# Performance work log

Hardware: AMD Instinct MI355X
Metric: run time of the kernel (lower is better)

## Reference

```python
import jax, jax.numpy as jnp
import numpy as np

# Mamba2 hyperparameters (from init_kwargs + mamba_ssm defaults)
D_MODEL = 1024
D_STATE = 64
D_CONV = 4
EXPAND = 2
HEADDIM = 64                      # mamba_ssm default
D_INNER = EXPAND * D_MODEL        # 2048
NHEADS = D_INNER // HEADDIM       # 32
NGROUPS = 1
CONV_DIM = D_INNER + 2 * NGROUPS * D_STATE      # 2176
D_IN_PROJ = 2 * D_INNER + 2 * NGROUPS * D_STATE + NHEADS  # 4256
BATCH, SEQLEN = 4, 2048


def setup_inputs() -> dict:
    key = jax.random.key(0)
    ks = jax.random.split(key, 8)
    x = jax.random.normal(ks[0], (BATCH, SEQLEN, D_MODEL), dtype=jnp.float32)
    W_in = jax.random.normal(ks[1], (D_MODEL, D_IN_PROJ), dtype=jnp.float32) * 0.02
    conv_w = jax.random.normal(ks[2], (CONV_DIM, D_CONV), dtype=jnp.float32) * 0.2
    conv_b = jnp.zeros((CONV_DIM,), dtype=jnp.float32)
    # dt_bias = inverse-softplus of dt ~ U(1e-3, 0.1), as in mamba_ssm init
    dt = jnp.exp(jax.random.uniform(ks[3], (NHEADS,)) * (np.log(0.1) - np.log(1e-3)) + np.log(1e-3))
    dt_bias = dt + jnp.log(-jnp.expm1(-dt))
    A_log = jnp.log(jax.random.uniform(ks[4], (NHEADS,), minval=1.0, maxval=16.0))
    D = jnp.ones((NHEADS,), dtype=jnp.float32)
    norm_w = jnp.ones((D_INNER,), dtype=jnp.float32)
    W_out = jax.random.normal(ks[5], (D_INNER, D_MODEL), dtype=jnp.float32) * 0.02
    return {"x": x, "W_in": W_in, "conv_w": conv_w, "conv_b": conv_b,
            "dt_bias": dt_bias, "A_log": A_log, "D": D, "norm_w": norm_w, "W_out": W_out}


def _mamba2_forward(x, W_in, conv_w, conv_b, dt_bias, A_log, D, norm_w, W_out):
    Bsz, L, _ = x.shape
    zxbcdt = x @ W_in                                   # [B, L, D_IN_PROJ]
    z = zxbcdt[..., :D_INNER]                           # gate
    xBC = zxbcdt[..., D_INNER:D_INNER + CONV_DIM]
    dt = zxbcdt[..., D_INNER + CONV_DIM:]               # [B, L, H]
    dt = jax.nn.softplus(dt + dt_bias)

    # causal depthwise conv1d over time, kernel width D_CONV
    xp = jnp.pad(xBC, ((0, 0), (D_CONV - 1, 0), (0, 0)))
    xc = sum(xp[:, k:k + L, :] * conv_w[:, k] for k in range(D_CONV))
    xBC = jax.nn.silu(xc + conv_b)

    xh = xBC[..., :D_INNER].reshape(Bsz, L, NHEADS, HEADDIM)   # [B,L,H,P]
    Bm = xBC[..., D_INNER:D_INNER + D_STATE]                   # [B,L,N] (ngroups=1)
    Cm = xBC[..., D_INNER + D_STATE:]                          # [B,L,N]
    A = -jnp.exp(A_log)                                        # [H]

    # selective SSM scan: h_t = h_{t-1}*exp(dt_t*A) + dt_t * x_t (outer) B_t ; y_t = C_t . h_t
    def step(h, inp):
        dt_t, x_t, B_t, C_t = inp                 # [B,H],[B,H,P],[B,N],[B,N]
        dA = jnp.exp(dt_t * A)                    # [B,H]
        h = h * dA[..., None, None] + (dt_t[..., None] * x_t)[..., None] * B_t[:, None, None, :]
        y_t = jnp.einsum('bhpn,bn->bhp', h, C_t)
        return h, y_t

    h0 = jnp.zeros((Bsz, NHEADS, HEADDIM, D_STATE), dtype=x.dtype)
    inputs = (jnp.moveaxis(dt, 1, 0), jnp.moveaxis(xh, 1, 0),
              jnp.moveaxis(Bm, 1, 0), jnp.moveaxis(Cm, 1, 0))
    _, ys = jax.lax.scan(step, h0, inputs)                     # [L,B,H,P]
    y = jnp.moveaxis(ys, 0, 1) + xh * D[None, None, :, None]   # skip term D*x
    y = y.reshape(Bsz, L, D_INNER)

    # gated RMSNorm: norm(y * silu(z)) * weight
    y = y * jax.nn.silu(z)
    y = y * jax.lax.rsqrt(jnp.mean(y * y, axis=-1, keepdims=True) + 1e-5) * norm_w
    return y @ W_out


def reference(x, W_in, conv_w, conv_b, dt_bias, A_log, D, norm_w, W_out):
    return _mamba2_forward(x, W_in, conv_w, conv_b, dt_bias, A_log, D, norm_w, W_out)
```

## Files before the change

kernel.cpp:

```cpp
#include <hip/hip_runtime.h>
#include <hip/hip_bf16.h>

#define B_SZ   4
#define SEQ    2048
#define DM     1024
#define DIN    2048
#define DST    64
#define NH     32
#define HD     64
#define CONVD  2176
#define DPROJ  4256
#define NPAD1  4352
#define MROWS  (B_SZ*SEQ)
#define QC     64
#define NC     (SEQ/QC)


typedef __attribute__((ext_vector_type(8))) __bf16 bf16x8;
typedef __attribute__((ext_vector_type(4))) __bf16 bf16x4;
typedef __attribute__((ext_vector_type(4))) float  floatx4;

__device__ __forceinline__ int swz(int row, int col) {
    return row * 64 + ((((col >> 3) ^ (row & 7)) << 3) | (col & 7));
}
__device__ __forceinline__ float bfbits2f(unsigned short u) {
    return __uint_as_float(((unsigned int)u) << 16);
}
__device__ __forceinline__ unsigned short f2bfbits(float f) {
    union { __bf16 h; unsigned short u; } cv; cv.h = (__bf16)f; return cv.u;
}

__global__ __launch_bounds__(256) void dtw_prep_kernel(const float* __restrict__ W_in,
                                                       float* __restrict__ dtWc) {
    int idx = blockIdx.x * 256 + threadIdx.x;
    int k = idx >> 5, h = idx & 31;
    dtWc[idx] = W_in[(size_t)k * DPROJ + 2 * DIN + 2 * DST + h];
}

__global__ __launch_bounds__(256) void cvt_dt_kernel(const float* __restrict__ x,
                                                     const float* __restrict__ dtWc,
                                                     __bf16* __restrict__ xbf,
                                                     float* __restrict__ dtraw) {
    __shared__ float xs[16][132];
    __shared__ float dtw[128 * 32];
    const int tid = threadIdx.x;
    const int r0 = blockIdx.x * 16;
    const int lm = tid & 15, pos = tid >> 4;
    const int rr = tid >> 4, h2 = (tid & 15) * 2;
    __bf16* slab = xbf + (size_t)blockIdx.x * (16 * DM);

    float a0 = 0.f, a1 = 0.f;
    for (int kc = 0; kc < 8; kc++) {
        #pragma unroll
        for (int i = 0; i < 2; i++) {
            int idx = tid + 256 * i;
            int row = idx >> 5, c4 = idx & 31;
            float4 v = ((const float4*)(x + (size_t)(r0 + row) * DM + kc * 128))[c4];
            xs[row][c4 * 4 + 0] = v.x; xs[row][c4 * 4 + 1] = v.y;
            xs[row][c4 * 4 + 2] = v.z; xs[row][c4 * 4 + 3] = v.w;
        }
        #pragma unroll
        for (int i = 0; i < 16; i++)
            dtw[tid + 256 * i] = dtWc[kc * 4096 + tid + 256 * i];
        __syncthreads();
        {
            bf16x8 o;
            #pragma unroll
            for (int e = 0; e < 8; e++) o[e] = (__bf16)xs[lm][pos * 8 + e];
            int kb = kc * 4 + (pos >> 2), q = pos & 3;
            *(bf16x8*)(slab + (size_t)(kb * 64 + q * 16 + lm) * 8) = o;
        }
        for (int j = 0; j < 128; j++) {
            float xv = xs[rr][j];
            a0 = fmaf(xv, dtw[j * 32 + h2], a0);
            a1 = fmaf(xv, dtw[j * 32 + h2 + 1], a1);
        }
        __syncthreads();
    }
    dtraw[(size_t)(r0 + rr) * NH + h2]     = a0;
    dtraw[(size_t)(r0 + rr) * NH + h2 + 1] = a1;
}

__global__ __launch_bounds__(256) void transpose_tiled_kernel(const float* __restrict__ src,
                                                              __bf16* __restrict__ dst,
                                                              int Ksrc, int Csrc) {
    __shared__ float tile[32][129];
    const int tid = threadIdx.x;
    const int mb = blockIdx.x, kb = blockIdx.y;
    const int K32 = Ksrc >> 5;
    #pragma unroll
    for (int i = 0; i < 4; i++) {
        int idx = tid + 256 * i;
        int kl = idx >> 5, c4 = idx & 31;
        int n = mb * 128 + c4 * 4;
        float4 v = make_float4(0.f, 0.f, 0.f, 0.f);
        if (n < Csrc) v = *(const float4*)(src + (size_t)(kb * 32 + kl) * Csrc + n);
        tile[kl][c4 * 4 + 0] = v.x; tile[kl][c4 * 4 + 1] = v.y;
        tile[kl][c4 * 4 + 2] = v.z; tile[kl][c4 * 4 + 3] = v.w;
    }
    __syncthreads();
    #pragma unroll
    for (int i = 0; i < 2; i++) {
        int c = tid + 256 * i;
        int sub = c >> 6, ln = c & 63, q = ln >> 4, lmn = ln & 15;
        bf16x8 o;
        #pragma unroll
        for (int e = 0; e < 8; e++) o[e] = (__bf16)tile[q * 8 + e][sub * 16 + lmn];
        *(bf16x8*)(dst + ((((size_t)(mb * 8 + sub)) * K32 + kb) << 9) + (ln << 3)) = o;
    }
}

template<int STORE_BF16>
__global__ __launch_bounds__(256) void gemm_tt_kernel(const __bf16* __restrict__ A,
                                                      const __bf16* __restrict__ Bt,
                                                      float* __restrict__ Cf,
                                                      __bf16* __restrict__ Cb,
                                                      int N, int K) {
    __shared__ __align__(16) __bf16 As[4096];
    __shared__ __align__(16) __bf16 Bs[4096];
    const int tid = threadIdx.x;
    const int wave = tid >> 6, lane = tid & 63;
    const int lm = lane & 15, lq = lane >> 4;
    const int mb = blockIdx.x, nb = blockIdx.y;
    const int K32 = K >> 5;

    floatx4 acc[4][4] = {};

    for (int kb = 0; kb < K32; kb++) {
        #pragma unroll
        for (int r = 0; r < 2; r++) {
            int c = tid + (r << 8);
            int sub = c >> 6, ln = c & 63;
            __builtin_amdgcn_global_load_lds(
                reinterpret_cast<const unsigned int*>(
                    A + ((((size_t)(mb * 8 + sub)) * K32 + kb) << 9) + (ln << 3)),
                reinterpret_cast<unsigned int*>(As + (size_t)c * 8), 16, 0, 0);
            __builtin_amdgcn_global_load_lds(
                reinterpret_cast<const unsigned int*>(
                    Bt + ((((size_t)(nb * 8 + sub)) * K32 + kb) << 9) + (ln << 3)),
                reinterpret_cast<unsigned int*>(Bs + (size_t)c * 8), 16, 0, 0);
        }
        __syncthreads();
        bf16x8 af[4], bfr[4];
        #pragma unroll
        for (int i = 0; i < 4; i++)
            af[i] = *(const bf16x8*)(As + ((((wave & 1) << 2) + i) << 9) + (lane << 3));
        #pragma unroll
        for (int i = 0; i < 4; i++)
            bfr[i] = *(const bf16x8*)(Bs + ((((wave >> 1) << 2) + i) << 9) + (lane << 3));
        #pragma unroll
        for (int mi = 0; mi < 4; mi++)
            #pragma unroll
            for (int ni = 0; ni < 4; ni++)
                acc[mi][ni] = __builtin_amdgcn_mfma_f32_16x16x32_bf16(af[mi], bfr[ni], acc[mi][ni], 0, 0, 0);
        __syncthreads();
    }

    const int wm = (wave & 1) << 6, wn = (wave >> 1) << 6;
    #pragma unroll
    for (int mi = 0; mi < 4; mi++) {
        #pragma unroll
        for (int r = 0; r < 4; r++) {
            int row = mb * 128 + wm + mi * 16 + lq * 4 + r;
            #pragma unroll
            for (int ni = 0; ni < 4; ni++) {
                int col = nb * 128 + wn + ni * 16 + lm;
                if (col < N) {
                    if (STORE_BF16) Cb[(size_t)row * N + col] = (__bf16)acc[mi][ni][r];
                    else            Cf[(size_t)row * N + col] = acc[mi][ni][r];
                }
            }
        }
    }
}

__global__ __launch_bounds__(256) void conv_silu_kernel(const __bf16* __restrict__ zx,
                                                        const float* __restrict__ cw,
                                                        const float* __restrict__ cb,
                                                        __bf16* __restrict__ out) {
    const int tid = threadIdx.x;
    const int tc = tid & 15, tt = tid >> 4;
    const int c0 = (blockIdx.x * 16 + tc) * 8;
    const int tg = blockIdx.y * 16 + tt;
    const int b = tg >> 8, t0 = (tg & 255) << 3;

    float xb[11][8];
    #pragma unroll
    for (int i = 0; i < 11; i++) {
        int t = t0 + i - 3;
        if (t >= 0) {
            bf16x8 v = *(const bf16x8*)(zx + ((size_t)(b * SEQ + t)) * DPROJ + DIN + c0);
            #pragma unroll
            for (int j = 0; j < 8; j++) xb[i][j] = (float)v[j];
        } else {
            #pragma unroll
            for (int j = 0; j < 8; j++) xb[i][j] = 0.f;
        }
    }
    float w0[8], w1[8], w2[8], w3[8], bias[8];
    #pragma unroll
    for (int j = 0; j < 8; j++) {
        float4 w = *(const float4*)(cw + (size_t)(c0 + j) * 4);
        w0[j] = w.x; w1[j] = w.y; w2[j] = w.z; w3[j] = w.w;
        bias[j] = cb[c0 + j];
    }
    #pragma unroll
    for (int s = 0; s < 8; s++) {
        bf16x8 o;
        #pragma unroll
        for (int j = 0; j < 8; j++) {
            float v = bias[j] + w0[j] * xb[s][j] + w1[j] * xb[s + 1][j]
                              + w2[j] * xb[s + 2][j] + w3[j] * xb[s + 3][j];
            o[j] = (__bf16)(v / (1.f + __expf(-v)));
        }
        *(bf16x8*)(out + ((size_t)(b * SEQ + t0 + s)) * CONVD + c0) = o;
    }
}

__global__ __launch_bounds__(256) void dt_prep_kernel(const float* __restrict__ dtraw,
                                                      const float* __restrict__ dt_bias,
                                                      const float* __restrict__ A_log,
                                                      float* __restrict__ dtv,
                                                      float* __restrict__ cum) {
    int blk = blockIdx.x;
    int b = blk >> 5, h = blk & 31;
    int wave = threadIdx.x >> 6, lane = threadIdx.x & 63;
    float Ah = -__expf(A_log[h]);
    float dtb = dt_bias[h];
    for (int c = wave; c < NC; c += 4) {
        int t = c * QC + lane;
        float u = dtraw[((size_t)b * SEQ + t) * NH + h] + dtb;
        float d = fmaxf(u, 0.f) + log1pf(__expf(-fabsf(u)));
        float s = d * Ah;
        #pragma unroll
        for (int o = 1; o < 64; o <<= 1) {
            float v = __shfl_up(s, o);
            if (lane >= o) s += v;
        }
        size_t idx = (size_t)blk * SEQ + t;
        dtv[idx] = d;
        cum[idx] = s;
    }
}

__global__ __launch_bounds__(256) void chunk_state_kernel(const __bf16* __restrict__ xc,
                                                          const float* __restrict__ dtv,
                                                          const float* __restrict__ cum,
                                                          __bf16* __restrict__ Sbuf) {
    const int blk = blockIdx.x;
    const int hq = blk & 7;
    const int bc = blk >> 3;
    const int c = bc & (NC - 1), b = bc >> 5;
    const int tid = threadIdx.x;
    const int wave = tid >> 6, lane = tid & 63;
    const int lm = lane & 15, q = lane >> 4;
    const int h = hq * 4 + wave;

    __shared__ __align__(16) __bf16 sBt[4096];
    __shared__ __align__(16) __bf16 sXw[4][4096];

    const size_t rowbase = (size_t)b * SEQ + (size_t)c * QC;
    {
        int k = tid & 31, n0 = (tid >> 5) * 8;
        unsigned short u0[8], u1[8];
        *(uint4*)u0 = *(const uint4*)(xc + (rowbase + 2 * k) * CONVD + DIN + n0);
        *(uint4*)u1 = *(const uint4*)(xc + (rowbase + 2 * k + 1) * CONVD + DIN + n0);
        #pragma unroll
        for (int i = 0; i < 8; i++) {
            unsigned int v = (unsigned int)u0[i] | ((unsigned int)u1[i] << 16);
            ((unsigned int*)sBt)[swz(n0 + i, 2 * k) >> 1] = v;
        }
    }
    const float* cump = cum + (size_t)(b * NH + h) * SEQ + (size_t)c * QC;
    const float* dtp  = dtv + (size_t)(b * NH + h) * SEQ + (size_t)c * QC;
    {
        int k = lane & 31, ph = (lane >> 5) * 32;
        float clast = cump[63];
        float w0 = dtp[2 * k]     * __expf(clast - cump[2 * k]);
        float w1 = dtp[2 * k + 1] * __expf(clast - cump[2 * k + 1]);
        unsigned short u0[32], u1[32];
        const __bf16* r0 = xc + (rowbase + 2 * k) * CONVD + h * 64 + ph;
        const __bf16* r1 = xc + (rowbase + 2 * k + 1) * CONVD + h * 64 + ph;
        #pragma unroll
        for (int i = 0; i < 4; i++) {
            ((uint4*)u0)[i] = ((const uint4*)r0)[i];
            ((uint4*)u1)[i] = ((const uint4*)r1)[i];
        }
        unsigned int* dstw = (unsigned int*)sXw[wave];
        #pragma unroll
        for (int i = 0; i < 32; i++) {
            unsigned int lo = f2bfbits(bfbits2f(u0[i]) * w0);
            unsigned int hi = f2bfbits(bfbits2f(u1[i]) * w1);
            dstw[swz(ph + i, 2 * k) >> 1] = lo | (hi << 16);
        }
    }
    __syncthreads();

    floatx4 acc[4][4] = {};
    #pragma unroll
    for (int kb = 0; kb < 2; kb++) {
        bf16x8 aX[4], bB[4];
        #pragma unroll
        for (int pi = 0; pi < 4; pi++)
            aX[pi] = *(const bf16x8*)(&sXw[wave][swz(pi * 16 + lm, kb * 32 + q * 8)]);
        #pragma unroll
        for (int ni = 0; ni < 4; ni++)
            bB[ni] = *(const bf16x8*)(&sBt[swz(ni * 16 + lm, kb * 32 + q * 8)]);
        #pragma unroll
        for (int pi = 0; pi < 4; pi++)
            #pragma unroll
            for (int ni = 0; ni < 4; ni++)
                acc[pi][ni] = __builtin_amdgcn_mfma_f32_16x16x32_bf16(aX[pi], bB[ni], acc[pi][ni], 0, 0, 0);
    }
    __bf16* Sp = Sbuf + ((size_t)(b * NC + c) * NH + h) * (HD * DST);
    #pragma unroll
    for (int pi = 0; pi < 4; pi++)
        #pragma unroll
        for (int r = 0; r < 4; r++) {
            int p = pi * 16 + q * 4 + r;
            #pragma unroll
            for (int ni = 0; ni < 4; ni++)
                Sp[p * 64 + ni * 16 + lm] = (__bf16)acc[pi][ni][r];
        }
}

__global__ __launch_bounds__(256) void state_scan_kernel(__bf16* __restrict__ Sbuf,
                                                         const float* __restrict__ cum) {
    int blk = blockIdx.x;
    int b = blk >> 5, h = blk & 31;
    int off = threadIdx.x * 16;
    float run[16];
    #pragma unroll
    for (int n = 0; n < 16; n++) run[n] = 0.f;
    for (int c = 0; c < NC; c++) {
        __bf16* Sp = Sbuf + ((size_t)(b * NC + c) * NH + h) * (HD * DST) + off;
        float tmp[16];
        #pragma unroll
        for (int n = 0; n < 16; n++) tmp[n] = (float)Sp[n];
        #pragma unroll
        for (int n = 0; n < 16; n++) Sp[n] = (__bf16)run[n];
        float P = __expf(cum[(size_t)blk * SEQ + c * QC + QC - 1]);
        #pragma unroll
        for (int n = 0; n < 16; n++) run[n] = fmaf(run[n], P, tmp[n]);
    }
}

__global__ __launch_bounds__(128) void chunk_out_kernel(const __bf16* __restrict__ xc,
                                                        const float* __restrict__ dtv,
                                                        const float* __restrict__ cum,
                                                        const __bf16* __restrict__ Sbuf,
                                                        const float* __restrict__ Dv,
                                                        __bf16* __restrict__ y) {
    const int blk = blockIdx.x;
    const int hp = blk & 15;
    const int bc = blk >> 4;
    const int c = bc & (NC - 1), b = bc >> 5;
    const int tid = threadIdx.x;
    const int wave = tid >> 6, lane = tid & 63;
    const int lm = lane & 15, q = lane >> 4;
    const int h = hp * 2 + wave;

    __shared__ __align__(16) __bf16 smem[16384];
    __bf16* sB  = smem;
    __bf16* sC  = smem + 4096;
    __bf16* sXt = smem + 8192 + (wave << 12);
    __bf16* sP  = smem + (wave << 12);

    const size_t rowbase = (size_t)b * SEQ + (size_t)c * QC;
    {
        int r = tid >> 1, c0 = (tid & 1) * 32;
        const __bf16* gB = xc + (rowbase + r) * CONVD + DIN + c0;
        const __bf16* gC = xc + (rowbase + r) * CONVD + DIN + DST + c0;
        #pragma unroll
        for (int i = 0; i < 4; i++) {
            *(uint4*)(&sB[swz(r, c0 + i * 8)]) = *(const uint4*)(gB + i * 8);
            *(uint4*)(&sC[swz(r, c0 + i * 8)]) = *(const uint4*)(gC + i * 8);
        }
    }
    {
        int k = lane & 31, ph = (lane >> 5) * 32;
        unsigned short u0[32], u1[32];
        const __bf16* r0 = xc + (rowbase + 2 * k) * CONVD + h * 64 + ph;
        const __bf16* r1 = xc + (rowbase + 2 * k + 1) * CONVD + h * 64 + ph;
        #pragma unroll
        for (int i = 0; i < 4; i++) {
            ((uint4*)u0)[i] = ((const uint4*)r0)[i];
            ((uint4*)u1)[i] = ((const uint4*)r1)[i];
        }
        unsigned int* dstw = (unsigned int*)sXt;
        #pragma unroll
        for (int i = 0; i < 32; i++)
            dstw[swz(ph + i, 2 * k) >> 1] = (unsigned int)u0[i] | ((unsigned int)u1[i] << 16);
    }
    __syncthreads();

    const float* cump = cum + (size_t)(b * NH + h) * SEQ + (size_t)c * QC;
    const float* dtp  = dtv + (size_t)(b * NH + h) * SEQ + (size_t)c * QC;
    float cumv = cump[lane], dtvv = dtp[lane];
    float ct[4][4];
    #pragma unroll
    for (int ti = 0; ti < 4; ti++)
        #pragma unroll
        for (int r = 0; r < 4; r++)
            ct[ti][r] = __shfl(cumv, ti * 16 + q * 4 + r);
    float cums_l[4], dtv_l[4];
    #pragma unroll
    for (int si = 0; si < 4; si++) {
        cums_l[si] = __shfl(cumv, si * 16 + lm);
        dtv_l[si]  = __shfl(dtvv, si * 16 + lm);
    }

    bf16x8 afC[4][2];
    #pragma unroll
    for (int ti = 0; ti < 4; ti++)
        #pragma unroll
        for (int kb = 0; kb < 2; kb++)
            afC[ti][kb] = *(const bf16x8*)(&sC[swz(ti * 16 + lm, kb * 32 + q * 8)]);

    floatx4 accG[4][4] = {};
    #pragma unroll
    for (int kb = 0; kb < 2; kb++) {
        bf16x8 bfB[4];
        #pragma unroll
        for (int si = 0; si < 4; si++)
            bfB[si] = *(const bf16x8*)(&sB[swz(si * 16 + lm, kb * 32 + q * 8)]);
        #pragma unroll
        for (int ti = 0; ti < 4; ti++)
            #pragma unroll
            for (int si = 0; si < 4; si++)
                if (si <= ti)
                    accG[ti][si] = __builtin_amdgcn_mfma_f32_16x16x32_bf16(afC[ti][kb], bfB[si], accG[ti][si], 0, 0, 0);
    }
    __syncthreads();

    float Dh = Dv[h];
    #pragma unroll
    for (int ti = 0; ti < 4; ti++)
        #pragma unroll
        for (int si = 0; si < 4; si++) {
            if (si > ti) continue;
            #pragma unroll
            for (int r = 0; r < 4; r++) {
                int t = ti * 16 + q * 4 + r;
                float arg = fminf(ct[ti][r] - cums_l[si], 0.f);
                float val = dtv_l[si] * __expf(arg) * accG[ti][si][r];
                if (ti == si) {
                    if (lm > q * 4 + r) val = 0.f;
                    else if (lm == q * 4 + r) val += Dh;
                }
                sP[swz(t, si * 16 + lm)] = (__bf16)val;
            }
        }
    #pragma unroll
    for (int r = 0; r < 4; r++) {
        sP[swz(q * 4 + r, 16 + lm)] = (__bf16)0.f;
        sP[swz(32 + q * 4 + r, 48 + lm)] = (__bf16)0.f;
    }
    __syncthreads();

    floatx4 accY[4][4] = {};
    const __bf16* Sp = Sbuf + ((size_t)(b * NC + c) * NH + h) * (HD * DST);
    #pragma unroll
    for (int kb = 0; kb < 2; kb++) {
        bf16x8 bS[4];
        #pragma unroll
        for (int pi = 0; pi < 4; pi++)
            bS[pi] = *(const bf16x8*)(Sp + (pi * 16 + lm) * 64 + kb * 32 + q * 8);
        #pragma unroll
        for (int ti = 0; ti < 4; ti++)
            #pragma unroll
            for (int pi = 0; pi < 4; pi++)
                accY[ti][pi] = __builtin_amdgcn_mfma_f32_16x16x32_bf16(afC[ti][kb], bS[pi], accY[ti][pi], 0, 0, 0);
    }
    #pragma unroll
    for (int ti = 0; ti < 4; ti++)
        #pragma unroll
        for (int r = 0; r < 4; r++) {
            float e = __expf(ct[ti][r]);
            #pragma unroll
            for (int pi = 0; pi < 4; pi++)
                accY[ti][pi][r] *= e;
        }

    #pragma unroll
    for (int kb = 0; kb < 2; kb++) {
        bf16x8 bX[4];
        #pragma unroll
        for (int pi = 0; pi < 4; pi++)
            bX[pi] = *(const bf16x8*)(&sXt[swz(pi * 16 + lm, kb * 32 + q * 8)]);
        #pragma unroll
        for (int ti = 0; ti < 4; ti++) {
            if (ti < 2 * kb) continue;
            bf16x8 aP = *(const bf16x8*)(&sP[swz(ti * 16 + lm, kb * 32 + q * 8)]);
            #pragma unroll
            for (int pi = 0; pi < 4; pi++)
                accY[ti][pi] = __builtin_amdgcn_mfma_f32_16x16x32_bf16(aP, bX[pi], accY[ti][pi], 0, 0, 0);
        }
    }

    const int R4v = (int)(rowbase >> 4);
    #pragma unroll
    for (int ti = 0; ti < 4; ti++) {
        __bf16* slab = y + (size_t)(R4v + ti) * 32768;
        #pragma unroll
        for (int pi = 0; pi < 4; pi++) {
            int kbC = h * 2 + (pi >> 1);
            int qC  = ((pi & 1) << 1) + (lm >> 3);
            int colpart = kbC * 512 + qC * 128 + (lm & 7);
            #pragma unroll
            for (int r = 0; r < 4; r++)
                slab[colpart + (q * 4 + r) * 8] = (__bf16)accY[ti][pi][r];
        }
    }
}

__global__ __launch_bounds__(256) void gate_norm_kernel(__bf16* __restrict__ y,
                                                        const __bf16* __restrict__ zx,
                                                        const float* __restrict__ nw) {
    const int tid = threadIdx.x;
    const int lm = tid & 15;
    __bf16* yfb = y + (size_t)blockIdx.x * 32768;
    const size_t zrow = ((size_t)blockIdx.x * 16 + lm) * DPROJ;

    float ss = 0.f;
    #pragma unroll
    for (int i = 0; i < 16; i++) {
        int g = tid + 256 * i;
        int pos = g >> 4;
        bf16x8 yv = *(const bf16x8*)(yfb + (size_t)g * 8);
        bf16x8 zv = *(const bf16x8*)(zx + zrow + pos * 8);
        #pragma unroll
        for (int j = 0; j < 8; j++) {
            float z = (float)zv[j];
            float val = (float)yv[j] * (z / (1.f + __expf(-z)));
            ss += val * val;
        }
    }
    __shared__ float red[16][16];
    __shared__ float sscale[16];
    red[lm][tid >> 4] = ss;
    __syncthreads();
    if (tid < 16) {
        float tot = 0.f;
        #pragma unroll
        for (int j = 0; j < 16; j++) tot += red[tid][j];
        sscale[tid] = rsqrtf(tot * (1.f / (float)DIN) + 1e-5f);
    }
    __syncthreads();
    float sc = sscale[lm];
    #pragma unroll
    for (int i = 0; i < 16; i++) {
        int g = tid + 256 * i;
        int pos = g >> 4;
        bf16x8 yv = *(const bf16x8*)(yfb + (size_t)g * 8);
        bf16x8 zv = *(const bf16x8*)(zx + zrow + pos * 8);
        float4 n0 = *(const float4*)(nw + pos * 8);
        float4 n1 = *(const float4*)(nw + pos * 8 + 4);
        float nwv[8] = {n0.x, n0.y, n0.z, n0.w, n1.x, n1.y, n1.z, n1.w};
        bf16x8 o;
        #pragma unroll
        for (int j = 0; j < 8; j++) {
            float z = (float)zv[j];
            float val = (float)yv[j] * (z / (1.f + __expf(-z)));
            o[j] = (__bf16)(val * sc * nwv[j]);
        }
        *(bf16x8*)(yfb + (size_t)g * 8) = o;
    }
}

extern "C" void kernel_launch(void* const* d_in, const int* in_sizes, int n_in,
                              void* d_out, int out_size, void* d_ws, size_t ws_size,
                              hipStream_t stream) {
    const float* x       = (const float*)d_in[0];
    const float* W_in    = (const float*)d_in[1];
    const float* conv_w  = (const float*)d_in[2];
    const float* conv_b  = (const float*)d_in[3];
    const float* dt_bias = (const float*)d_in[4];
    const float* A_log   = (const float*)d_in[5];
    const float* Dv      = (const float*)d_in[6];
    const float* norm_w  = (const float*)d_in[7];
    const float* W_out   = (const float*)d_in[8];
    float* out = (float*)d_out;

    char* ws = (char*)d_ws;
    size_t off = 0;
    auto take = [&](size_t bytes) { void* p = ws + off; off = (off + bytes + 255) & ~(size_t)255; return p; };
    __bf16* xbf    = (__bf16*)take((size_t)MROWS * DM * 2);
    __bf16* WinT   = (__bf16*)take((size_t)NPAD1 * DM * 2);
    __bf16* WoutT  = (__bf16*)take((size_t)DM * DIN * 2);
    __bf16* zx     = (__bf16*)take((size_t)MROWS * DPROJ * 2);
    __bf16* xc     = (__bf16*)take((size_t)MROWS * CONVD * 2);
    __bf16* yf     = (__bf16*)take((size_t)MROWS * DIN * 2);
    float*  dtraw  = (float*) take((size_t)MROWS * NH * 4);
    float*  dtv    = (float*) take((size_t)B_SZ * NH * SEQ * 4);
    float*  cum    = (float*) take((size_t)B_SZ * NH * SEQ * 4);
    __bf16* Sbuf   = (__bf16*)take((size_t)B_SZ * NC * NH * HD * DST * 2);
    float*  dtWc   = (float*) take((size_t)DM * NH * 4);
    (void)ws_size;

    dtw_prep_kernel<<<dim3(DM * NH / 256), 256, 0, stream>>>(W_in, dtWc);
    cvt_dt_kernel<<<dim3(MROWS / 16), 256, 0, stream>>>(x, dtWc, xbf, dtraw);
    transpose_tiled_kernel<<<dim3(NPAD1 / 128, DM / 32), 256, 0, stream>>>(W_in, WinT, DM, DPROJ);
    transpose_tiled_kernel<<<dim3(DM / 128, DIN / 32), 256, 0, stream>>>(W_out, WoutT, DIN, DM);
    gemm_tt_kernel<1><<<dim3(MROWS / 128, NPAD1 / 128), 256, 0, stream>>>(
        xbf, WinT, nullptr, zx, DPROJ, DM);
    conv_silu_kernel<<<dim3(17, 64), 256, 0, stream>>>(zx, conv_w, conv_b, xc);
    dt_prep_kernel<<<dim3(B_SZ * NH), 256, 0, stream>>>(dtraw, dt_bias, A_log, dtv, cum);
    chunk_state_kernel<<<dim3(B_SZ * NC * (NH / 4)), 256, 0, stream>>>(xc, dtv, cum, Sbuf);
    state_scan_kernel<<<dim3(B_SZ * NH), 256, 0, stream>>>(Sbuf, cum);
    chunk_out_kernel<<<dim3(B_SZ * NC * (NH / 2)), 128, 0, stream>>>(xc, dtv, cum, Sbuf, Dv, yf);
    gate_norm_kernel<<<dim3(MROWS / 16), 256, 0, stream>>>(yf, zx, norm_w);
    gemm_tt_kernel<0><<<dim3(MROWS / 128, DM / 128), 256, 0, stream>>>(
        yf, WoutT, out, nullptr, DM, DIN);
}
```

Before: 402.9 us.

## Fuse gated RMSNorm into chunk output and GEMM epilogue, merge prep kernels

Removes the separate gate_norm pass. chunk_out now applies silu(z) gating, writes the gated y, and atomically accumulates per-row sums of squares. The output GEMM epilogue applies the rsqrt row scale, and norm_w is folded into the transposed W_out during weight prep. The two weight transposes and the dt-weight extraction become one kernel, conv and dt_prep merge into one launch that also zeroes rowsum, and the in_proj GEMM drops the dt columns (N 4352→4224), since dt is already computed separately. state_scan splits each head across 4 blocks with vectorized bf16x4 access. The cost is atomics and uncoalesced z reads in chunk_out.

Result: faster. 379.6 us (-5.8%).

```diff
diff --git a/kernel.cpp b/kernel.cpp
--- a/kernel.cpp
+++ b/kernel.cpp
@@ -10,7 +10,7 @@
 #define HD     64
 #define CONVD  2176
 #define DPROJ  4256
-#define NPAD1  4352
+#define NPROJ  4224
 #define MROWS  (B_SZ*SEQ)
 #define QC     64
 #define NC     (SEQ/QC)
@@ -30,11 +30,50 @@
     union { __bf16 h; unsigned short u; } cv; cv.h = (__bf16)f; return cv.u;
 }
 
-__global__ __launch_bounds__(256) void dtw_prep_kernel(const float* __restrict__ W_in,
-                                                       float* __restrict__ dtWc) {
-    int idx = blockIdx.x * 256 + threadIdx.x;
-    int k = idx >> 5, h = idx & 31;
-    dtWc[idx] = W_in[(size_t)k * DPROJ + 2 * DIN + 2 * DST + h];
+__global__ __launch_bounds__(256) void prep_weights_kernel(const float* __restrict__ W_in,
+                                                           const float* __restrict__ W_out,
+                                                           const float* __restrict__ norm_w,
+                                                           float* __restrict__ dtWc,
+                                                           __bf16* __restrict__ WinT,
+                                                           __bf16* __restrict__ WoutT) {
+    __shared__ float tile[32][129];
+    const int bid = blockIdx.x, tid = threadIdx.x;
+    if (bid < 128) {
+        int idx = bid * 256 + tid;
+        int k = idx >> 5, h = idx & 31;
+        dtWc[idx] = W_in[(size_t)k * DPROJ + 2 * DIN + 2 * DST + h];
+        return;
+    }
+    const float* src; __bf16* dst; const float* scal; int Ksrc, Csrc, mb, kb;
+    if (bid < 128 + 1056) {
+        int t = bid - 128; mb = t >> 5; kb = t & 31;
+        src = W_in; dst = WinT; scal = nullptr; Ksrc = DM; Csrc = DPROJ;
+    } else {
+        int t = bid - 1184; mb = t >> 6; kb = t & 63;
+        src = W_out; dst = WoutT; scal = norm_w; Ksrc = DIN; Csrc = DM;
+    }
+    const int K32 = Ksrc >> 5;
+    #pragma unroll
+    for (int i = 0; i < 4; i++) {
+        int idx = tid + 256 * i;
+        int kl = idx >> 5, c4 = idx & 31;
+        int n = mb * 128 + c4 * 4;
+        float4 v = make_float4(0.f, 0.f, 0.f, 0.f);
+        if (n < Csrc) v = *(const float4*)(src + (size_t)(kb * 32 + kl) * Csrc + n);
+        if (scal) { float s = scal[kb * 32 + kl]; v.x *= s; v.y *= s; v.z *= s; v.w *= s; }
+        tile[kl][c4 * 4 + 0] = v.x; tile[kl][c4 * 4 + 1] = v.y;
+        tile[kl][c4 * 4 + 2] = v.z; tile[kl][c4 * 4 + 3] = v.w;
+    }
+    __syncthreads();
+    #pragma unroll
+    for (int i = 0; i < 2; i++) {
+        int c = tid + 256 * i;
+        int sub = c >> 6, ln = c & 63, q = ln >> 4, lmn = ln & 15;
+        bf16x8 o;
+        #pragma unroll
+        for (int e = 0; e < 8; e++) o[e] = (__bf16)tile[q * 8 + e][sub * 16 + lmn];
+        *(bf16x8*)(dst + ((((size_t)(mb * 8 + sub)) * K32 + kb) << 9) + (ln << 3)) = o;
+    }
 }
 
 __global__ __launch_bounds__(256) void cvt_dt_kernel(const float* __restrict__ x,
@@ -81,40 +120,12 @@
     dtraw[(size_t)(r0 + rr) * NH + h2 + 1] = a1;
 }
 
-__global__ __launch_bounds__(256) void transpose_tiled_kernel(const float* __restrict__ src,
-                                                              __bf16* __restrict__ dst,
-                                                              int Ksrc, int Csrc) {
-    __shared__ float tile[32][129];
-    const int tid = threadIdx.x;
-    const int mb = blockIdx.x, kb = blockIdx.y;
-    const int K32 = Ksrc >> 5;
-    #pragma unroll
-    for (int i = 0; i < 4; i++) {
-        int idx = tid + 256 * i;
-        int kl = idx >> 5, c4 = idx & 31;
-        int n = mb * 128 + c4 * 4;
-        float4 v = make_float4(0.f, 0.f, 0.f, 0.f);
-        if (n < Csrc) v = *(const float4*)(src + (size_t)(kb * 32 + kl) * Csrc + n);
-        tile[kl][c4 * 4 + 0] = v.x; tile[kl][c4 * 4 + 1] = v.y;
-        tile[kl][c4 * 4 + 2] = v.z; tile[kl][c4 * 4 + 3] = v.w;
-    }
-    __syncthreads();
-    #pragma unroll
-    for (int i = 0; i < 2; i++) {
-        int c = tid + 256 * i;
-        int sub = c >> 6, ln = c & 63, q = ln >> 4, lmn = ln & 15;
-        bf16x8 o;
-        #pragma unroll
-        for (int e = 0; e < 8; e++) o[e] = (__bf16)tile[q * 8 + e][sub * 16 + lmn];
-        *(bf16x8*)(dst + ((((size_t)(mb * 8 + sub)) * K32 + kb) << 9) + (ln << 3)) = o;
-    }
-}
-
 template<int STORE_BF16>
 __global__ __launch_bounds__(256) void gemm_tt_kernel(const __bf16* __restrict__ A,
                                                       const __bf16* __restrict__ Bt,
                                                       float* __restrict__ Cf,
                                                       __bf16* __restrict__ Cb,
+                                                      const float* __restrict__ rowscale,
                                                       int N, int K) {
     __shared__ __align__(16) __bf16 As[4096];
     __shared__ __align__(16) __bf16 Bs[4096];
@@ -162,84 +173,92 @@
         #pragma unroll
         for (int r = 0; r < 4; r++) {
             int row = mb * 128 + wm + mi * 16 + lq * 4 + r;
+            float s = 1.f;
+            if (rowscale) s = rsqrtf(rowscale[row] * (1.f / (float)DIN) + 1e-5f);
             #pragma unroll
             for (int ni = 0; ni < 4; ni++) {
                 int col = nb * 128 + wn + ni * 16 + lm;
                 if (col < N) {
                     if (STORE_BF16) Cb[(size_t)row * N + col] = (__bf16)acc[mi][ni][r];
-                    else            Cf[(size_t)row * N + col] = acc[mi][ni][r];
+                    else            Cf[(size_t)row * N + col] = acc[mi][ni][r] * s;
                 }
             }
         }
     }
 }
 
-__global__ __launch_bounds__(256) void conv_silu_kernel(const __bf16* __restrict__ zx,
-                                                        const float* __restrict__ cw,
-                                                        const float* __restrict__ cb,
-                                                        __bf16* __restrict__ out) {
-    const int tid = threadIdx.x;
-    const int tc = tid & 15, tt = tid >> 4;
-    const int c0 = (blockIdx.x * 16 + tc) * 8;
-    const int tg = blockIdx.y * 16 + tt;
-    const int b = tg >> 8, t0 = (tg & 255) << 3;
-
-    float xb[11][8];
-    #pragma unroll
-    for (int i = 0; i < 11; i++) {
-        int t = t0 + i - 3;
-        if (t >= 0) {
-            bf16x8 v = *(const bf16x8*)(zx + ((size_t)(b * SEQ + t)) * DPROJ + DIN + c0);
-            #pragma unroll
-            for (int j = 0; j < 8; j++) xb[i][j] = (float)v[j];
-        } else {
-            #pragma unroll
-            for (int j = 0; j < 8; j++) xb[i][j] = 0.f;
-        }
-    }
-    float w0[8], w1[8], w2[8], w3[8], bias[8];
-    #pragma unroll
-    for (int j = 0; j < 8; j++) {
-        float4 w = *(const float4*)(cw + (size_t)(c0 + j) * 4);
-        w0[j] = w.x; w1[j] = w.y; w2[j] = w.z; w3[j] = w.w;
-        bias[j] = cb[c0 + j];
-    }
-    #pragma unroll
-    for (int s = 0; s < 8; s++) {
-        bf16x8 o;
-        #pragma unroll
-        for (int j = 0; j < 8; j++) {
-            float v = bias[j] + w0[j] * xb[s][j] + w1[j] * xb[s + 1][j]
-                              + w2[j] * xb[s + 2][j] + w3[j] * xb[s + 3][j];
-            o[j] = (__bf16)(v / (1.f + __expf(-v)));
-        }
-        *(bf16x8*)(out + ((size_t)(b * SEQ + t0 + s)) * CONVD + c0) = o;
-    }
-}
-
-__global__ __launch_bounds__(256) void dt_prep_kernel(const float* __restrict__ dtraw,
+__global__ __launch_bounds__(256) void conv_dt_kernel(const __bf16* __restrict__ zx,
+                                                      const float* __restrict__ cw,
+                                                      const float* __restrict__ cb,
+                                                      __bf16* __restrict__ out,
+                                                      const float* __restrict__ dtraw,
                                                       const float* __restrict__ dt_bias,
                                                       const float* __restrict__ A_log,
                                                       float* __restrict__ dtv,
-                                                      float* __restrict__ cum) {
-    int blk = blockIdx.x;
-    int b = blk >> 5, h = blk & 31;
-    int wave = threadIdx.x >> 6, lane = threadIdx.x & 63;
-    float Ah = -__expf(A_log[h]);
-    float dtb = dt_bias[h];
-    for (int c = wave; c < NC; c += 4) {
-        int t = c * QC + lane;
-        float u = dtraw[((size_t)b * SEQ + t) * NH + h] + dtb;
-        float d = fmaxf(u, 0.f) + log1pf(__expf(-fabsf(u)));
-        float s = d * Ah;
-        #pragma unroll
-        for (int o = 1; o < 64; o <<= 1) {
-            float v = __shfl_up(s, o);
-            if (lane >= o) s += v;
-        }
-        size_t idx = (size_t)blk * SEQ + t;
-        dtv[idx] = d;
-        cum[idx] = s;
+                                                      float* __restrict__ cum,
+                                                      float* __restrict__ rowsum) {
+    const int bid = blockIdx.x, tid = threadIdx.x;
+    if (bid < 1088) {
+        const int by = bid / 17, bx = bid - by * 17;
+        const int tc = tid & 15, tt = tid >> 4;
+        const int c0 = (bx * 16 + tc) * 8;
+        const int tg = by * 16 + tt;
+        const int b = tg >> 8, t0 = (tg & 255) << 3;
+
+        float xb[11][8];
+        #pragma unroll
+        for (int i = 0; i < 11; i++) {
+            int t = t0 + i - 3;
+            if (t >= 0) {
+                bf16x8 v = *(const bf16x8*)(zx + ((size_t)(b * SEQ + t)) * NPROJ + DIN + c0);
+                #pragma unroll
+                for (int j = 0; j < 8; j++) xb[i][j] = (float)v[j];
+            } else {
+                #pragma unroll
+                for (int j = 0; j < 8; j++) xb[i][j] = 0.f;
+            }
+        }
+        float w0[8], w1[8], w2[8], w3[8], bias[8];
+        #pragma unroll
+        for (int j = 0; j < 8; j++) {
+            float4 w = *(const float4*)(cw + (size_t)(c0 + j) * 4);
+            w0[j] = w.x; w1[j] = w.y; w2[j] = w.z; w3[j] = w.w;
+            bias[j] = cb[c0 + j];
+        }
+        #pragma unroll
+        for (int s = 0; s < 8; s++) {
+            bf16x8 o;
+            #pragma unroll
+            for (int j = 0; j < 8; j++) {
+                float v = bias[j] + w0[j] * xb[s][j] + w1[j] * xb[s + 1][j]
+                                  + w2[j] * xb[s + 2][j] + w3[j] * xb[s + 3][j];
+                o[j] = (__bf16)(v / (1.f + __expf(-v)));
+            }
+            *(bf16x8*)(out + ((size_t)(b * SEQ + t0 + s)) * CONVD + c0) = o;
+        }
+    } else if (bid < 1216) {
+        const int blk = bid - 1088;
+        const int b = blk >> 5, h = blk & 31;
+        const int wave = tid >> 6, lane = tid & 63;
+        float Ah = -__expf(A_log[h]);
+        float dtb = dt_bias[h];
+        for (int c = wave; c < NC; c += 4) {
+            int t = c * QC + lane;
+            float u = dtraw[((size_t)b * SEQ + t) * NH + h] + dtb;
+            float d = fmaxf(u, 0.f) + log1pf(__expf(-fabsf(u)));
+            float s = d * Ah;
+            #pragma unroll
+            for (int o = 1; o < 64; o <<= 1) {
+                float v = __shfl_up(s, o);
+                if (lane >= o) s += v;
+            }
+            size_t idx = (size_t)blk * SEQ + t;
+            dtv[idx] = d;
+            cum[idx] = s;
+        }
+    } else {
+        float4 z = make_float4(0.f, 0.f, 0.f, 0.f);
+        *(float4*)(rowsum + (size_t)(bid - 1216) * 1024 + tid * 4) = z;
     }
 }
 
@@ -326,22 +345,26 @@
 
 __global__ __launch_bounds__(256) void state_scan_kernel(__bf16* __restrict__ Sbuf,
                                                          const float* __restrict__ cum) {
-    int blk = blockIdx.x;
+    int blk = blockIdx.x >> 2;
+    int part = blockIdx.x & 3;
     int b = blk >> 5, h = blk & 31;
-    int off = threadIdx.x * 16;
-    float run[16];
-    #pragma unroll
-    for (int n = 0; n < 16; n++) run[n] = 0.f;
+    int off = part * 1024 + threadIdx.x * 4;
+    float run[4];
+    #pragma unroll
+    for (int n = 0; n < 4; n++) run[n] = 0.f;
     for (int c = 0; c < NC; c++) {
         __bf16* Sp = Sbuf + ((size_t)(b * NC + c) * NH + h) * (HD * DST) + off;
-        float tmp[16];
-        #pragma unroll
-        for (int n = 0; n < 16; n++) tmp[n] = (float)Sp[n];
-        #pragma unroll
-        for (int n = 0; n < 16; n++) Sp[n] = (__bf16)run[n];
+        bf16x4 sv = *(const bf16x4*)Sp;
+        float tmp[4];
+        #pragma unroll
+        for (int n = 0; n < 4; n++) tmp[n] = (float)sv[n];
+        bf16x4 ov;
+        #pragma unroll
+        for (int n = 0; n < 4; n++) ov[n] = (__bf16)run[n];
+        *(bf16x4*)Sp = ov;
         float P = __expf(cum[(size_t)blk * SEQ + c * QC + QC - 1]);
         #pragma unroll
-        for (int n = 0; n < 16; n++) run[n] = fmaf(run[n], P, tmp[n]);
+        for (int n = 0; n < 4; n++) run[n] = fmaf(run[n], P, tmp[n]);
     }
 }
 
@@ -350,6 +373,8 @@
                                                         const float* __restrict__ cum,
                                                         const __bf16* __restrict__ Sbuf,
                                                         const float* __restrict__ Dv,
+                                                        const __bf16* __restrict__ zx,
+                                                        float* __restrict__ rowsum,
                                                         __bf16* __restrict__ y) {
     const int blk = blockIdx.x;
     const int hp = blk & 15;
@@ -503,68 +528,25 @@
     for (int ti = 0; ti < 4; ti++) {
         __bf16* slab = y + (size_t)(R4v + ti) * 32768;
         #pragma unroll
-        for (int pi = 0; pi < 4; pi++) {
-            int kbC = h * 2 + (pi >> 1);
-            int qC  = ((pi & 1) << 1) + (lm >> 3);
-            int colpart = kbC * 512 + qC * 128 + (lm & 7);
-            #pragma unroll
-            for (int r = 0; r < 4; r++)
-                slab[colpart + (q * 4 + r) * 8] = (__bf16)accY[ti][pi][r];
-        }
-    }
-}
-
-__global__ __launch_bounds__(256) void gate_norm_kernel(__bf16* __restrict__ y,
-                                                        const __bf16* __restrict__ zx,
-                                                        const float* __restrict__ nw) {
-    const int tid = threadIdx.x;
-    const int lm = tid & 15;
-    __bf16* yfb = y + (size_t)blockIdx.x * 32768;
-    const size_t zrow = ((size_t)blockIdx.x * 16 + lm) * DPROJ;
-
-    float ss = 0.f;
-    #pragma unroll
-    for (int i = 0; i < 16; i++) {
-        int g = tid + 256 * i;
-        int pos = g >> 4;
-        bf16x8 yv = *(const bf16x8*)(yfb + (size_t)g * 8);
-        bf16x8 zv = *(const bf16x8*)(zx + zrow + pos * 8);
-        #pragma unroll
-        for (int j = 0; j < 8; j++) {
-            float z = (float)zv[j];
-            float val = (float)yv[j] * (z / (1.f + __expf(-z)));
-            ss += val * val;
-        }
-    }
-    __shared__ float red[16][16];
-    __shared__ float sscale[16];
-    red[lm][tid >> 4] = ss;
-    __syncthreads();
-    if (tid < 16) {
-        float tot = 0.f;
-        #pragma unroll
-        for (int j = 0; j < 16; j++) tot += red[tid][j];
-        sscale[tid] = rsqrtf(tot * (1.f / (float)DIN) + 1e-5f);
-    }
-    __syncthreads();
-    float sc = sscale[lm];
-    #pragma unroll
-    for (int i = 0; i < 16; i++) {
-        int g = tid + 256 * i;
-        int pos = g >> 4;
-        bf16x8 yv = *(const bf16x8*)(yfb + (size_t)g * 8);
-        bf16x8 zv = *(const bf16x8*)(zx + zrow + pos * 8);
-        float4 n0 = *(const float4*)(nw + pos * 8);
-        float4 n1 = *(const float4*)(nw + pos * 8 + 4);
-        float nwv[8] = {n0.x, n0.y, n0.z, n0.w, n1.x, n1.y, n1.z, n1.w};
-        bf16x8 o;
-        #pragma unroll
-        for (int j = 0; j < 8; j++) {
-            float z = (float)zv[j];
-            float val = (float)yv[j] * (z / (1.f + __expf(-z)));
-            o[j] = (__bf16)(val * sc * nwv[j]);
-        }
-        *(bf16x8*)(yfb + (size_t)g * 8) = o;
+        for (int r = 0; r < 4; r++) {
+            int t = ti * 16 + q * 4 + r;
+            const __bf16* zrow = zx + (rowbase + t) * NPROJ + h * 64;
+            float rs = 0.f;
+            #pragma unroll
+            for (int pi = 0; pi < 4; pi++) {
+                float zv = (float)zrow[pi * 16 + lm];
+                float g = accY[ti][pi][r] * (zv / (1.f + __expf(-zv)));
+                rs += g * g;
+                int kbC = h * 2 + (pi >> 1);
+                int qC  = ((pi & 1) << 1) + (lm >> 3);
+                slab[kbC * 512 + qC * 128 + (lm & 7) + (q * 4 + r) * 8] = (__bf16)g;
+            }
+            rs += __shfl_xor(rs, 1);
+            rs += __shfl_xor(rs, 2);
+            rs += __shfl_xor(rs, 4);
+            rs += __shfl_xor(rs, 8);
+            if (lm == 0) atomicAdd(&rowsum[rowbase + t], rs);
+        }
     }
 }
 
@@ -586,9 +568,9 @@
     size_t off = 0;
     auto take = [&](size_t bytes) { void* p = ws + off; off = (off + bytes + 255) & ~(size_t)255; return p; };
     __bf16* xbf    = (__bf16*)take((size_t)MROWS * DM * 2);
-    __bf16* WinT   = (__bf16*)take((size_t)NPAD1 * DM * 2);
+    __bf16* WinT   = (__bf16*)take((size_t)NPROJ * DM * 2);
     __bf16* WoutT  = (__bf16*)take((size_t)DM * DIN * 2);
-    __bf16* zx     = (__bf16*)take((size_t)MROWS * DPROJ * 2);
+    __bf16* zx     = (__bf16*)take((size_t)MROWS * NPROJ * 2);
     __bf16* xc     = (__bf16*)take((size_t)MROWS * CONVD * 2);
     __bf16* yf     = (__bf16*)take((size_t)MROWS * DIN * 2);
     float*  dtraw  = (float*) take((size_t)MROWS * NH * 4);
@@ -596,20 +578,19 @@
     float*  cum    = (float*) take((size_t)B_SZ * NH * SEQ * 4);
     __bf16* Sbuf   = (__bf16*)take((size_t)B_SZ * NC * NH * HD * DST * 2);
     float*  dtWc   = (float*) take((size_t)DM * NH * 4);
+    float*  rowsum = (float*) take((size_t)MROWS * 4);
     (void)ws_size;
 
-    dtw_prep_kernel<<<dim3(DM * NH / 256), 256, 0, stream>>>(W_in, dtWc);
+    prep_weights_kernel<<<dim3(1696), 256, 0, stream>>>(W_in, W_out, norm_w, dtWc, WinT, WoutT);
     cvt_dt_kernel<<<dim3(MROWS / 16), 256, 0, stream>>>(x, dtWc, xbf, dtraw);
-    transpose_tiled_kernel<<<dim3(NPAD1 / 128, DM / 32), 256, 0, stream>>>(W_in, WinT, DM, DPROJ);
-    transpose_tiled_kernel<<<dim3(DM / 128, DIN / 32), 256, 0, stream>>>(W_out, WoutT, DIN, DM);
-    gemm_tt_kernel<1><<<dim3(MROWS / 128, NPAD1 / 128), 256, 0, stream>>>(
-        xbf, WinT, nullptr, zx, DPROJ, DM);
-    conv_silu_kernel<<<dim3(17, 64), 256, 0, stream>>>(zx, conv_w, conv_b, xc);
-    dt_prep_kernel<<<dim3(B_SZ * NH), 256, 0, stream>>>(dtraw, dt_bias, A_log, dtv, cum);
+    gemm_tt_kernel<1><<<dim3(MROWS / 128, NPROJ / 128), 256, 0, stream>>>(
+        xbf, WinT, nullptr, zx, nullptr, NPROJ, DM);
+    conv_dt_kernel<<<dim3(1224), 256, 0, stream>>>(zx, conv_w, conv_b, xc,
+                                                   dtraw, dt_bias, A_log, dtv, cum, rowsum);
     chunk_state_kernel<<<dim3(B_SZ * NC * (NH / 4)), 256, 0, stream>>>(xc, dtv, cum, Sbuf);
-    state_scan_kernel<<<dim3(B_SZ * NH), 256, 0, stream>>>(Sbuf, cum);
-    chunk_out_kernel<<<dim3(B_SZ * NC * (NH / 2)), 128, 0, stream>>>(xc, dtv, cum, Sbuf, Dv, yf);
-    gate_norm_kernel<<<dim3(MROWS / 16), 256, 0, stream>>>(yf, zx, norm_w);
+    state_scan_kernel<<<dim3(B_SZ * NH * 4), 256, 0, stream>>>(Sbuf, cum);
+    chunk_out_kernel<<<dim3(B_SZ * NC * (NH / 2)), 128, 0, stream>>>(
+        xc, dtv, cum, Sbuf, Dv, zx, rowsum, yf);
     gemm_tt_kernel<0><<<dim3(MROWS / 128, DM / 128), 256, 0, stream>>>(
-        yf, WoutT, out, nullptr, DM, DIN);
-}
+        yf, WoutT, out, nullptr, rowsum, DM, DIN);
+}
```
